# Kernel tuning notes

Hardware: AMD Instinct MI355X
Metric: run time of the kernel (lower is better)

The kernel has to match this reference:

```python
import jax, jax.numpy as jnp
import numpy as np

EPS = 1e-5

def _bn(x, g, b, m, v):
    return (x - m) * jax.lax.rsqrt(v + EPS) * g + b

def _lrelu(x):
    return jnp.where(x >= 0, x, 0.2 * x)

def setup_inputs() -> dict:
    key = jax.random.key(0)
    B, N, K, Cg, Cin, Cn, Cout = 4, 8192, 16, 10, 128, 128, 256
    ks = jax.random.split(key, 8)
    d = {
        "feature": jax.random.normal(ks[0], (B, N, Cin), jnp.float32),
        "raw_neighbors_feature": jax.random.normal(ks[1], (B, N, K, Cg), jnp.float32),
        "neighbors_idx": jax.random.randint(ks[2], (B, N, K), 0, N, jnp.int64),
        "w_n": jax.random.normal(ks[3], (Cg, Cn), jnp.float32) * (1.0 / np.sqrt(Cg)),
        "b_n": jnp.zeros((Cn,), jnp.float32),
        "g_n": jnp.ones((Cn,), jnp.float32),
        "beta_n": jnp.zeros((Cn,), jnp.float32),
        "rm_n": jnp.zeros((Cn,), jnp.float32),
        "rv_n": jnp.ones((Cn,), jnp.float32),
        "w_attn": jax.random.normal(ks[4], (Cin + Cn, Cin + Cn), jnp.float32) * (1.0 / np.sqrt(Cin + Cn)),
        "w_o": jax.random.normal(ks[5], (Cin + Cn, Cout), jnp.float32) * (1.0 / np.sqrt(Cin + Cn)),
        "b_o": jnp.zeros((Cout,), jnp.float32),
        "g_o": jnp.ones((Cout,), jnp.float32),
        "beta_o": jnp.zeros((Cout,), jnp.float32),
        "rm_o": jnp.zeros((Cout,), jnp.float32),
        "rv_o": jnp.ones((Cout,), jnp.float32),
        "w_s": jax.random.normal(ks[6], (Cin, Cout), jnp.float32) * (1.0 / np.sqrt(Cin)),
        "b_s": jnp.zeros((Cout,), jnp.float32),
        "g_s": jnp.ones((Cout,), jnp.float32),
        "beta_s": jnp.zeros((Cout,), jnp.float32),
        "rm_s": jnp.zeros((Cout,), jnp.float32),
        "rv_s": jnp.ones((Cout,), jnp.float32),
    }
    return d

def reference(feature, raw_neighbors_feature, neighbors_idx,
              w_n, b_n, g_n, beta_n, rm_n, rv_n,
              w_attn,
              w_o, b_o, g_o, beta_o, rm_o, rv_o,
              w_s, b_s, g_s, beta_s, rm_s, rv_s):
    # mlp_neighbor_fea: Linear + BN1d + leaky_relu(0.2) on raw neighbor features [B,N,K,Cg]->[B,N,K,Cn]
    neigh = _lrelu(_bn(raw_neighbors_feature @ w_n + b_n, g_n, beta_n, rm_n, rv_n))
    # index_points: gather per-point neighbor features [B,N,K,Cin]
    gathered = jax.vmap(lambda f, i: f[i])(feature, neighbors_idx)
    cat = jnp.concatenate([gathered, neigh], axis=-1)  # [B,N,K,Cin+Cn]
    # attn_pooling: softmax over neighbor axis K, weighted sum
    attn = jax.nn.softmax(cat @ w_attn, axis=2)
    pooled = jnp.sum(attn * cat, axis=2)  # [B,N,Cin+Cn]
    # shortcut + out MLPs (Linear + BN, no activation) then leaky_relu(0.2)
    out = _lrelu(_bn(feature @ w_s + b_s, g_s, beta_s, rm_s, rv_s)
                 + _bn(pooled @ w_o + b_o, g_o, beta_o, rm_o, rv_o))
    return out
```

## Files before the change

kernel.cpp:

```cpp
#include <hip/hip_runtime.h>
#include <hip/hip_bf16.h>

typedef __attribute__((ext_vector_type(8))) short bf16x8;
typedef __attribute__((ext_vector_type(4))) float f32x4;
typedef __attribute__((ext_vector_type(16))) float f32x16;

#define NPTS 8192
#define KNB  16
#define CG   10
#define CIN  128
#define CC   256
#define COUT 256
#define PB   8
#define A2_LD 400

#define WSA_OFF 0
#define WSB_OFF 131072
#define DD_OFF  327680
#define WN_OFF  328704
#define DN_OFF  336896
#define FB_OFF  524288
#define WS_FB   (FB_OFF + 8388608ull)

#define LOG2E 1.4426950408889634f

__device__ __forceinline__ short f2bs(float x) {
    __hip_bfloat16 h = __float2bfloat16(x);
    return *reinterpret_cast<short*>(&h);
}

__global__ __launch_bounds__(256) void lfa_pre(
    const float* __restrict__ feature,
    const float* __restrict__ w_attn,
    const float* __restrict__ w_n, const float* __restrict__ b_n,
    const float* __restrict__ g_n, const float* __restrict__ beta_n,
    const float* __restrict__ rm_n, const float* __restrict__ rv_n,
    const float* __restrict__ w_o, const float* __restrict__ b_o,
    const float* __restrict__ g_o, const float* __restrict__ beta_o,
    const float* __restrict__ rm_o, const float* __restrict__ rv_o,
    const float* __restrict__ w_s, const float* __restrict__ b_s,
    const float* __restrict__ g_s, const float* __restrict__ beta_s,
    const float* __restrict__ rm_s, const float* __restrict__ rv_s,
    __hip_bfloat16* __restrict__ featbf,
    __hip_bfloat16* __restrict__ wsA, __hip_bfloat16* __restrict__ wsB,
    float* __restrict__ dd,
    __hip_bfloat16* __restrict__ wsN, float* __restrict__ dnw,
    int use_fb)
{
    const int b = blockIdx.x, tid = threadIdx.x;
    if (b < 2048) {
        if (!use_fb) return;
        size_t gid = (size_t)b * 256 + tid;
        const float4* src = (const float4*)(feature + gid * 8);
        float4 x = src[0], y = src[1];
        bf16x8 v;
        v[0] = f2bs(x.x); v[1] = f2bs(x.y); v[2] = f2bs(x.z); v[3] = f2bs(x.w);
        v[4] = f2bs(y.x); v[5] = f2bs(y.y); v[6] = f2bs(y.z); v[7] = f2bs(y.w);
        *(bf16x8*)(featbf + gid * 8) = v;
        return;
    }
    int gid = (b - 2048) * 256 + tid;
    if (gid < 8192) {
        int f = gid >> 6, l = gid & 63;
        int kt = f >> 3, nt = f & 7, hi = l >> 5, c5 = l & 31;
        int col = nt * 32 + c5;
        bf16x8 v;
        #pragma unroll
        for (int j = 0; j < 8; ++j)
            v[j] = f2bs(w_attn[(kt * 16 + hi * 8 + j) * CC + col] * LOG2E);
        *(bf16x8*)(wsA + (size_t)gid * 8) = v;
    } else if (gid < 8192 + 12288) {
        int g2 = gid - 8192;
        int f = g2 >> 6, l = g2 & 63;
        int kt = f >> 4, nt = f & 15, q = l >> 4, c0 = l & 15;
        int c = nt * 16 + c0;
        float as = g_s[c] * rsqrtf(rv_s[c] + 1e-5f);
        float ao = g_o[c] * rsqrtf(rv_o[c] + 1e-5f);
        bf16x8 v;
        #pragma unroll
        for (int j = 0; j < 8; ++j) {
            int r = kt * 32 + q * 8 + j;
            float x = (r < CIN) ? w_s[r * COUT + c] * as
                                : w_o[(r - CIN) * COUT + c] * ao;
            v[j] = f2bs(x);
        }
        *(bf16x8*)(wsB + (size_t)g2 * 8) = v;
    } else if (gid < 20736) {
        int c = gid - 20480;
        float as = g_s[c] * rsqrtf(rv_s[c] + 1e-5f);
        float ao = g_o[c] * rsqrtf(rv_o[c] + 1e-5f);
        dd[c] = beta_s[c] + (b_s[c] - rm_s[c]) * as
              + beta_o[c] + (b_o[c] - rm_o[c]) * ao;
    } else if (gid < 21248) {
        int g3 = gid - 20736;
        int nt = g3 >> 6, l = g3 & 63;
        int q = l >> 4, c0 = l & 15;
        int n = nt * 16 + c0;
        float an = g_n[n] * rsqrtf(rv_n[n] + 1e-5f);
        bf16x8 v;
        #pragma unroll
        for (int j = 0; j < 8; ++j) {
            int k = q * 8 + j;
            v[j] = (k < CG) ? f2bs(w_n[k * 128 + n] * an) : (short)0;
        }
        *(bf16x8*)(wsN + (size_t)g3 * 8) = v;
    } else if (gid < 21376) {
        int c = gid - 21248;
        float an = g_n[c] * rsqrtf(rv_n[c] + 1e-5f);
        dnw[c] = beta_n[c] + (b_n[c] - rm_n[c]) * an;
    }
}

__global__ __launch_bounds__(512, 4) void lfa_main(
    const float* __restrict__ feature,
    const float* __restrict__ rawn,
    const int*   __restrict__ nidx,
    const __hip_bfloat16* __restrict__ wsA,
    const __hip_bfloat16* __restrict__ wsB,
    const float* __restrict__ dd,
    const __hip_bfloat16* __restrict__ wsN,
    const float* __restrict__ dnw,
    const __hip_bfloat16* __restrict__ featbf,
    int use_fb,
    float* __restrict__ out)
{
    __shared__ __align__(16) __hip_bfloat16 catS[128 * 256];
    __shared__ __align__(16) __hip_bfloat16 a2S[PB * A2_LD];

    const int tid  = threadIdx.x;
    const int lane = tid & 63;
    const int w    = tid >> 6;
    const int q    = lane >> 4;
    const int c0   = lane & 15;
    const int hi   = lane >> 5;
    const int c5   = lane & 31;
    const long long base0 = (long long)blockIdx.x * PB;
    const long long bIdx  = base0 >> 13;

    bf16x8 am;
    {
        bf16x8 v;
        #pragma unroll
        for (int j = 0; j < 8; ++j) v[j] = 0;
        const float* rb = rawn + ((base0 + w) * KNB + c0) * CG;
        if (q == 0) {
            float2 a0 = *(const float2*)(rb + 0), a1 = *(const float2*)(rb + 2);
            float2 a2 = *(const float2*)(rb + 4), a3 = *(const float2*)(rb + 6);
            v[0] = f2bs(a0.x); v[1] = f2bs(a0.y); v[2] = f2bs(a1.x); v[3] = f2bs(a1.y);
            v[4] = f2bs(a2.x); v[5] = f2bs(a2.y); v[6] = f2bs(a3.x); v[7] = f2bs(a3.y);
        } else if (q == 1) {
            float2 a4 = *(const float2*)(rb + 8);
            v[0] = f2bs(a4.x); v[1] = f2bs(a4.y);
        }
        am = v;
    }

    if (use_fb) {
        if (tid < 128) {
            int p = tid >> 4, ch = tid & 15;
            *(bf16x8*)&a2S[p * A2_LD + ch * 8] =
                *(const bf16x8*)(featbf + (base0 + p) * CIN + ch * 8);
        }
    } else {
        int p = tid >> 6, cc = (tid & 63) * 2;
        const float* src = feature + (base0 + p) * CIN + cc;
        a2S[p * A2_LD + cc]     = __float2bfloat16(src[0]);
        a2S[p * A2_LD + cc + 1] = __float2bfloat16(src[1]);
    }
    {
        int row = tid >> 2, qd = tid & 3;
        int ridx = nidx[base0 * KNB + row];
        int sw = row & 7;
        if (use_fb) {
            const bf16x8* src = (const bf16x8*)(featbf + (bIdx * NPTS + ridx) * CIN + qd * 32);
            #pragma unroll
            for (int j = 0; j < 4; ++j)
                *(bf16x8*)&catS[row * 256 + (((qd * 4 + j) ^ sw) << 3)] = src[j];
        } else {
            const float4* src = (const float4*)(feature + (bIdx * NPTS + ridx) * CIN + qd * 32);
            #pragma unroll
            for (int j = 0; j < 4; ++j) {
                float4 x = src[2 * j], y = src[2 * j + 1];
                bf16x8 v;
                v[0] = f2bs(x.x); v[1] = f2bs(x.y); v[2] = f2bs(x.z); v[3] = f2bs(x.w);
                v[4] = f2bs(y.x); v[5] = f2bs(y.y); v[6] = f2bs(y.z); v[7] = f2bs(y.w);
                *(bf16x8*)&catS[row * 256 + (((qd * 4 + j) ^ sw) << 3)] = v;
            }
        }
    }

    {
        const f32x4 vz = {0.f, 0.f, 0.f, 0.f};
        #pragma unroll
        for (int nt = 0; nt < 8; ++nt) {
            bf16x8 wnb = *(const bf16x8*)(wsN + (size_t)((nt * 64 + lane) * 8));
            f32x4 cm = __builtin_amdgcn_mfma_f32_16x16x32_bf16(am, wnb, vz, 0, 0, 0);
            int c = nt * 16 + c0;
            float dnv = dnw[c];
            int col = CIN + c;
            #pragma unroll
            for (int r = 0; r < 4; ++r) {
                float y = cm[r] + dnv;
                y = (y >= 0.f) ? y : 0.2f * y;
                int row = w * 16 + q * 4 + r;
                catS[row * 256 + ((((col >> 3) ^ (row & 7)) << 3)) + (col & 7)] =
                    __float2bfloat16(y);
            }
        }
    }
    __syncthreads();

    f32x16 acc32[4];
    #pragma unroll
    for (int m = 0; m < 4; ++m)
        #pragma unroll
        for (int r = 0; r < 16; ++r) acc32[m][r] = 0.f;

    #pragma unroll
    for (int kt = 0; kt < 16; ++kt) {
        bf16x8 bfr = *(const bf16x8*)(wsA + (size_t)(((kt * 8 + w) * 64 + lane) * 8));
        #pragma unroll
        for (int m = 0; m < 4; ++m) {
            int row = m * 32 + c5;
            int chunk = (kt * 2 + hi) ^ (row & 7);
            bf16x8 af = *(const bf16x8*)&catS[row * 256 + (chunk << 3)];
            acc32[m] = __builtin_amdgcn_mfma_f32_32x32x16_bf16(af, bfr, acc32[m], 0, 0, 0);
        }
    }

    {
        const int c = w * 32 + c5;
        int cvo4[4];
        #pragma unroll
        for (int rr = 0; rr < 4; ++rr)
            cvo4[rr] = ((((c >> 3) ^ (rr + 4 * hi)) << 3) + (c & 7));
        #pragma unroll
        for (int m = 0; m < 4; ++m) {
            float sA = 0.f, sB = 0.f, pA = 0.f, pB = 0.f;
            #pragma unroll
            for (int reg = 0; reg < 16; ++reg) {
                float e = __builtin_amdgcn_exp2f(acc32[m][reg]);
                int rowin = (reg & 3) + 8 * (reg >> 2) + 4 * hi;
                float cv = __bfloat162float(catS[(m * 32 + rowin) * 256 + cvo4[reg & 3]]);
                if (reg < 8) { sA += e; pA += e * cv; }
                else         { sB += e; pB += e * cv; }
            }
            sA += __shfl_xor(sA, 32);
            sB += __shfl_xor(sB, 32);
            pA += __shfl_xor(pA, 32);
            pB += __shfl_xor(pB, 32);
            if (hi == 0)
                a2S[(2 * m) * A2_LD + CIN + c] =
                    __float2bfloat16(pA * __builtin_amdgcn_rcpf(sA));
            else
                a2S[(2 * m + 1) * A2_LD + CIN + c] =
                    __float2bfloat16(pB * __builtin_amdgcn_rcpf(sB));
        }
    }
    __syncthreads();

    const f32x4 vzero = {0.f, 0.f, 0.f, 0.f};
    f32x4 acc2[2];
    acc2[0] = vzero; acc2[1] = vzero;
    #pragma unroll
    for (int kt = 0; kt < 12; ++kt) {
        bf16x8 a = *(const bf16x8*)&a2S[(c0 & 7) * A2_LD + kt * 32 + q * 8];
        bf16x8 b0 = *(const bf16x8*)(wsB + (size_t)(((kt * 16 + 2 * w + 0) * 64 + lane) * 8));
        bf16x8 b1 = *(const bf16x8*)(wsB + (size_t)(((kt * 16 + 2 * w + 1) * 64 + lane) * 8));
        acc2[0] = __builtin_amdgcn_mfma_f32_16x16x32_bf16(a, b0, acc2[0], 0, 0, 0);
        acc2[1] = __builtin_amdgcn_mfma_f32_16x16x32_bf16(a, b1, acc2[1], 0, 0, 0);
    }
    float* outS = (float*)catS;
    if (q < 2) {
        #pragma unroll
        for (int i = 0; i < 2; ++i) {
            int c = (2 * w + i) * 16 + c0;
            float dv = dd[c];
            #pragma unroll
            for (int r = 0; r < 4; ++r) {
                int p = q * 4 + r;
                float y = acc2[i][r] + dv;
                y = (y >= 0.f) ? y : 0.2f * y;
                outS[p * 256 + c] = y;
            }
        }
    }
    __syncthreads();
    {
        int p = tid >> 6, c4 = (tid & 63) * 4;
        *(float4*)(out + (base0 + p) * COUT + c4) = *(const float4*)&outS[p * 256 + c4];
    }
}

extern "C" void kernel_launch(void* const* d_in, const int* in_sizes, int n_in,
                              void* d_out, int out_size, void* d_ws, size_t ws_size,
                              hipStream_t stream) {
    const float* feature = (const float*)d_in[0];
    const float* rawn    = (const float*)d_in[1];
    const int*   nidx    = (const int*)d_in[2];
    const float* w_n     = (const float*)d_in[3];
    const float* b_n     = (const float*)d_in[4];
    const float* g_n     = (const float*)d_in[5];
    const float* beta_n  = (const float*)d_in[6];
    const float* rm_n    = (const float*)d_in[7];
    const float* rv_n    = (const float*)d_in[8];
    const float* w_attn  = (const float*)d_in[9];
    const float* w_o     = (const float*)d_in[10];
    const float* b_o     = (const float*)d_in[11];
    const float* g_o     = (const float*)d_in[12];
    const float* beta_o  = (const float*)d_in[13];
    const float* rm_o    = (const float*)d_in[14];
    const float* rv_o    = (const float*)d_in[15];
    const float* w_s     = (const float*)d_in[16];
    const float* b_s     = (const float*)d_in[17];
    const float* g_s     = (const float*)d_in[18];
    const float* beta_s  = (const float*)d_in[19];
    const float* rm_s    = (const float*)d_in[20];
    const float* rv_s    = (const float*)d_in[21];
    float* out = (float*)d_out;

    __hip_bfloat16* wsA    = (__hip_bfloat16*)((char*)d_ws + WSA_OFF);
    __hip_bfloat16* wsB    = (__hip_bfloat16*)((char*)d_ws + WSB_OFF);
    float*          ddp    = (float*)((char*)d_ws + DD_OFF);
    __hip_bfloat16* wsN    = (__hip_bfloat16*)((char*)d_ws + WN_OFF);
    float*          dnw    = (float*)((char*)d_ws + DN_OFF);
    __hip_bfloat16* featbf = (__hip_bfloat16*)((char*)d_ws + FB_OFF);
    const int use_fb = (ws_size >= WS_FB) ? 1 : 0;

    lfa_pre<<<2132, 256, 0, stream>>>(
        feature, w_attn,
        w_n, b_n, g_n, beta_n, rm_n, rv_n,
        w_o, b_o, g_o, beta_o, rm_o, rv_o,
        w_s, b_s, g_s, beta_s, rm_s, rv_s,
        featbf, wsA, wsB, ddp, wsN, dnw, use_fb);

    const int nblocks = (4 * NPTS) / PB;
    lfa_main<<<nblocks, 512, 0, stream>>>(
        feature, rawn, nidx,
        wsA, wsB, ddp, wsN, dnw, featbf, use_fb, out);
}
```

Measured before the change: 237.2 us.

## Drop bf16 feature precast and retile attention GEMM into 2x2 wave tiles

Removes the pre-pass that converted the whole feature tensor to bf16 in workspace. The main kernel now always gathers fp32 neighbor rows and converts them on the fly, which shrinks the prep launch but doubles the bytes each gather reads. The attention-logit GEMM is reorganized so each wave computes a 2x2 block of 32x32 tiles instead of a 4x1 column strip. This halves the LDS A-fragment reads per MFMA at the cost of one extra weight load per k-step.

```diff
diff --git a/kernel.cpp b/kernel.cpp
--- a/kernel.cpp
+++ b/kernel.cpp
@@ -19,8 +19,6 @@
 #define DD_OFF  327680
 #define WN_OFF  328704
 #define DN_OFF  336896
-#define FB_OFF  524288
-#define WS_FB   (FB_OFF + 8388608ull)
 
 #define LOG2E 1.4426950408889634f
 
@@ -30,7 +28,6 @@
 }
 
 __global__ __launch_bounds__(256) void lfa_pre(
-    const float* __restrict__ feature,
     const float* __restrict__ w_attn,
     const float* __restrict__ w_n, const float* __restrict__ b_n,
     const float* __restrict__ g_n, const float* __restrict__ beta_n,
@@ -41,25 +38,11 @@
     const float* __restrict__ w_s, const float* __restrict__ b_s,
     const float* __restrict__ g_s, const float* __restrict__ beta_s,
     const float* __restrict__ rm_s, const float* __restrict__ rv_s,
-    __hip_bfloat16* __restrict__ featbf,
     __hip_bfloat16* __restrict__ wsA, __hip_bfloat16* __restrict__ wsB,
     float* __restrict__ dd,
-    __hip_bfloat16* __restrict__ wsN, float* __restrict__ dnw,
-    int use_fb)
+    __hip_bfloat16* __restrict__ wsN, float* __restrict__ dnw)
 {
-    const int b = blockIdx.x, tid = threadIdx.x;
-    if (b < 2048) {
-        if (!use_fb) return;
-        size_t gid = (size_t)b * 256 + tid;
-        const float4* src = (const float4*)(feature + gid * 8);
-        float4 x = src[0], y = src[1];
-        bf16x8 v;
-        v[0] = f2bs(x.x); v[1] = f2bs(x.y); v[2] = f2bs(x.z); v[3] = f2bs(x.w);
-        v[4] = f2bs(y.x); v[5] = f2bs(y.y); v[6] = f2bs(y.z); v[7] = f2bs(y.w);
-        *(bf16x8*)(featbf + gid * 8) = v;
-        return;
-    }
-    int gid = (b - 2048) * 256 + tid;
+    int gid = blockIdx.x * 256 + threadIdx.x;
     if (gid < 8192) {
         int f = gid >> 6, l = gid & 63;
         int kt = f >> 3, nt = f & 7, hi = l >> 5, c5 = l & 31;
@@ -120,8 +103,6 @@
     const float* __restrict__ dd,
     const __hip_bfloat16* __restrict__ wsN,
     const float* __restrict__ dnw,
-    const __hip_bfloat16* __restrict__ featbf,
-    int use_fb,
     float* __restrict__ out)
 {
     __shared__ __align__(16) __hip_bfloat16 catS[128 * 256];
@@ -130,6 +111,8 @@
     const int tid  = threadIdx.x;
     const int lane = tid & 63;
     const int w    = tid >> 6;
+    const int g    = w >> 2;
+    const int wg   = w & 3;
     const int q    = lane >> 4;
     const int c0   = lane & 15;
     const int hi   = lane >> 5;
@@ -155,13 +138,7 @@
         am = v;
     }
 
-    if (use_fb) {
-        if (tid < 128) {
-            int p = tid >> 4, ch = tid & 15;
-            *(bf16x8*)&a2S[p * A2_LD + ch * 8] =
-                *(const bf16x8*)(featbf + (base0 + p) * CIN + ch * 8);
-        }
-    } else {
+    {
         int p = tid >> 6, cc = (tid & 63) * 2;
         const float* src = feature + (base0 + p) * CIN + cc;
         a2S[p * A2_LD + cc]     = __float2bfloat16(src[0]);
@@ -171,21 +148,14 @@
         int row = tid >> 2, qd = tid & 3;
         int ridx = nidx[base0 * KNB + row];
         int sw = row & 7;
-        if (use_fb) {
-            const bf16x8* src = (const bf16x8*)(featbf + (bIdx * NPTS + ridx) * CIN + qd * 32);
-            #pragma unroll
-            for (int j = 0; j < 4; ++j)
-                *(bf16x8*)&catS[row * 256 + (((qd * 4 + j) ^ sw) << 3)] = src[j];
-        } else {
-            const float4* src = (const float4*)(feature + (bIdx * NPTS + ridx) * CIN + qd * 32);
-            #pragma unroll
-            for (int j = 0; j < 4; ++j) {
-                float4 x = src[2 * j], y = src[2 * j + 1];
-                bf16x8 v;
-                v[0] = f2bs(x.x); v[1] = f2bs(x.y); v[2] = f2bs(x.z); v[3] = f2bs(x.w);
-                v[4] = f2bs(y.x); v[5] = f2bs(y.y); v[6] = f2bs(y.z); v[7] = f2bs(y.w);
-                *(bf16x8*)&catS[row * 256 + (((qd * 4 + j) ^ sw) << 3)] = v;
-            }
+        const float4* src = (const float4*)(feature + (bIdx * NPTS + ridx) * CIN + qd * 32);
+        #pragma unroll
+        for (int j = 0; j < 4; ++j) {
+            float4 x = src[2 * j], y = src[2 * j + 1];
+            bf16x8 v;
+            v[0] = f2bs(x.x); v[1] = f2bs(x.y); v[2] = f2bs(x.z); v[3] = f2bs(x.w);
+            v[4] = f2bs(y.x); v[5] = f2bs(y.y); v[6] = f2bs(y.z); v[7] = f2bs(y.w);
+            *(bf16x8*)&catS[row * 256 + (((qd * 4 + j) ^ sw) << 3)] = v;
         }
     }
 
@@ -210,38 +180,41 @@
     }
     __syncthreads();
 
-    f32x16 acc32[4];
+    f32x16 acc32[2][2];
     #pragma unroll
-    for (int m = 0; m < 4; ++m)
-        #pragma unroll
-        for (int r = 0; r < 16; ++r) acc32[m][r] = 0.f;
+    for (int mm = 0; mm < 2; ++mm)
+        #pragma unroll
+        for (int i = 0; i < 2; ++i)
+            #pragma unroll
+            for (int r = 0; r < 16; ++r) acc32[mm][i][r] = 0.f;
 
     #pragma unroll
     for (int kt = 0; kt < 16; ++kt) {
-        bf16x8 bfr = *(const bf16x8*)(wsA + (size_t)(((kt * 8 + w) * 64 + lane) * 8));
-        #pragma unroll
-        for (int m = 0; m < 4; ++m) {
-            int row = m * 32 + c5;
+        bf16x8 bfr0 = *(const bf16x8*)(wsA + (size_t)(((kt * 8 + 2 * wg + 0) * 64 + lane) * 8));
+        bf16x8 bfr1 = *(const bf16x8*)(wsA + (size_t)(((kt * 8 + 2 * wg + 1) * 64 + lane) * 8));
+        #pragma unroll
+        for (int mm = 0; mm < 2; ++mm) {
+            int row = (2 * g + mm) * 32 + c5;
             int chunk = (kt * 2 + hi) ^ (row & 7);
             bf16x8 af = *(const bf16x8*)&catS[row * 256 + (chunk << 3)];
-            acc32[m] = __builtin_amdgcn_mfma_f32_32x32x16_bf16(af, bfr, acc32[m], 0, 0, 0);
-        }
-    }
-
-    {
-        const int c = w * 32 + c5;
-        int cvo4[4];
-        #pragma unroll
-        for (int rr = 0; rr < 4; ++rr)
-            cvo4[rr] = ((((c >> 3) ^ (rr + 4 * hi)) << 3) + (c & 7));
-        #pragma unroll
-        for (int m = 0; m < 4; ++m) {
+            acc32[mm][0] = __builtin_amdgcn_mfma_f32_32x32x16_bf16(af, bfr0, acc32[mm][0], 0, 0, 0);
+            acc32[mm][1] = __builtin_amdgcn_mfma_f32_32x32x16_bf16(af, bfr1, acc32[mm][1], 0, 0, 0);
+        }
+    }
+
+    #pragma unroll
+    for (int mm = 0; mm < 2; ++mm) {
+        int mt = 2 * g + mm;
+        #pragma unroll
+        for (int i = 0; i < 2; ++i) {
+            int c = (2 * wg + i) * 32 + c5;
             float sA = 0.f, sB = 0.f, pA = 0.f, pB = 0.f;
             #pragma unroll
             for (int reg = 0; reg < 16; ++reg) {
-                float e = __builtin_amdgcn_exp2f(acc32[m][reg]);
+                float e = __builtin_amdgcn_exp2f(acc32[mm][i][reg]);
                 int rowin = (reg & 3) + 8 * (reg >> 2) + 4 * hi;
-                float cv = __bfloat162float(catS[(m * 32 + rowin) * 256 + cvo4[reg & 3]]);
+                int cvo = ((((c >> 3) ^ ((reg & 3) + 4 * hi)) << 3) + (c & 7));
+                float cv = __bfloat162float(catS[(mt * 32 + rowin) * 256 + cvo]);
                 if (reg < 8) { sA += e; pA += e * cv; }
                 else         { sB += e; pB += e * cv; }
             }
@@ -250,10 +223,10 @@
             pA += __shfl_xor(pA, 32);
             pB += __shfl_xor(pB, 32);
             if (hi == 0)
-                a2S[(2 * m) * A2_LD + CIN + c] =
+                a2S[(2 * mt) * A2_LD + CIN + c] =
                     __float2bfloat16(pA * __builtin_amdgcn_rcpf(sA));
             else
-                a2S[(2 * m + 1) * A2_LD + CIN + c] =
+                a2S[(2 * mt + 1) * A2_LD + CIN + c] =
                     __float2bfloat16(pB * __builtin_amdgcn_rcpf(sB));
         }
     }
@@ -319,23 +292,21 @@
     const float* rv_s    = (const float*)d_in[21];
     float* out = (float*)d_out;
 
-    __hip_bfloat16* wsA    = (__hip_bfloat16*)((char*)d_ws + WSA_OFF);
-    __hip_bfloat16* wsB    = (__hip_bfloat16*)((char*)d_ws + WSB_OFF);
-    float*          ddp    = (float*)((char*)d_ws + DD_OFF);
-    __hip_bfloat16* wsN    = (__hip_bfloat16*)((char*)d_ws + WN_OFF);
-    float*          dnw    = (float*)((char*)d_ws + DN_OFF);
-    __hip_bfloat16* featbf = (__hip_bfloat16*)((char*)d_ws + FB_OFF);
-    const int use_fb = (ws_size >= WS_FB) ? 1 : 0;
-
-    lfa_pre<<<2132, 256, 0, stream>>>(
-        feature, w_attn,
+    __hip_bfloat16* wsA = (__hip_bfloat16*)((char*)d_ws + WSA_OFF);
+    __hip_bfloat16* wsB = (__hip_bfloat16*)((char*)d_ws + WSB_OFF);
+    float*          ddp = (float*)((char*)d_ws + DD_OFF);
+    __hip_bfloat16* wsN = (__hip_bfloat16*)((char*)d_ws + WN_OFF);
+    float*          dnw = (float*)((char*)d_ws + DN_OFF);
+
+    lfa_pre<<<84, 256, 0, stream>>>(
+        w_attn,
         w_n, b_n, g_n, beta_n, rm_n, rv_n,
         w_o, b_o, g_o, beta_o, rm_o, rv_o,
         w_s, b_s, g_s, beta_s, rm_s, rv_s,
-        featbf, wsA, wsB, ddp, wsN, dnw, use_fb);
+        wsA, wsB, ddp, wsN, dnw);
 
     const int nblocks = (4 * NPTS) / PB;
     lfa_main<<<nblocks, 512, 0, stream>>>(
         feature, rawn, nidx,
-        wsA, wsB, ddp, wsN, dnw, featbf, use_fb, out);
+        wsA, wsB, ddp, wsN, dnw, out);
 }
```

After: 266.4 us. +12.3%, slower.
